# Optimization experiments

Measured on AMD Instinct MI355X. Metric: run time of the kernel, lower is better.

## Reference

```python
import jax, jax.numpy as jnp
import numpy as np

N1, E1 = 102400, 300000
N2, E2 = 10240, 40960
N3, E3 = 1024, 4096
G = 64
D = 256   # node_dim == hidden_dim (forced by where(M==0, x, M))
B = 64    # bond_dim
DEPTHS = (3, 3, 4)


def _make_edges(rng, n_nodes, n_edges):
    # build mirrored directed edges so every edge has an exact reverse
    half = n_edges // 2
    u = rng.integers(0, n_nodes, half)
    v = rng.integers(0, n_nodes, half)
    src = np.concatenate([u, v])
    dst = np.concatenate([v, u])
    rev = np.concatenate([np.arange(half, n_edges), np.arange(0, half)])
    return np.stack([src, dst]).astype(np.int64), rev.astype(np.int64)


def _linear_params(key, fan_in, fan_out):
    k1, k2 = jax.random.split(key)
    s = 1.0 / np.sqrt(fan_in)
    W = jax.random.uniform(k1, (fan_in, fan_out), jnp.float32, -s, s)
    b = jax.random.uniform(k2, (fan_out,), jnp.float32, -s, s)
    return W, b


def setup_inputs() -> dict:
    rng = np.random.default_rng(0)
    key = jax.random.key(0)
    ks = jax.random.split(key, 16)

    ei1, rev1 = _make_edges(rng, N1, E1)
    ei2, rev2 = _make_edges(rng, N2, E2)
    ei3, rev3 = _make_edges(rng, N3, E3)

    inp = {
        "x": jax.random.normal(ks[0], (N1, D), jnp.float32),
        "edge_attr1": jax.random.normal(ks[1], (E1, B), jnp.float32),
        "edge_attr2": jax.random.normal(ks[2], (E2, B), jnp.float32),
        "edge_attr3": jax.random.normal(ks[3], (E3, B), jnp.float32),
        "edge_index1": jnp.asarray(ei1), "rev_edge_index1": jnp.asarray(rev1),
        "edge_index2": jnp.asarray(ei2), "rev_edge_index2": jnp.asarray(rev2),
        "edge_index3": jnp.asarray(ei3), "rev_edge_index3": jnp.asarray(rev3),
        "batch1_2": jnp.asarray(np.repeat(np.arange(N2), N1 // N2)),
        "batch2": jnp.asarray(np.repeat(np.arange(N3), N2 // N3)),
        "batch3": jnp.asarray(np.repeat(np.arange(G), N3 // G)),
    }
    kidx = 4
    for lvl in (1, 2, 3):
        Wi, bi = _linear_params(ks[kidx], D + B, D); kidx += 1
        Wh, bh = _linear_params(ks[kidx], D, D); kidx += 1
        Wo, bo = _linear_params(ks[kidx], D + D, D); kidx += 1
        inp[f"Wi{lvl}"], inp[f"bi{lvl}"] = Wi, bi
        inp[f"Wh{lvl}"], inp[f"bh{lvl}"] = Wh, bh
        inp[f"Wo{lvl}"], inp[f"bo{lvl}"] = Wo, bo
    return inp


def _bmp(x, src, dst, rev, ea, Wi, bi, Wh, bh, Wo, bo, depth):
    # BondMessagePassing.forward (dropout is identity in eval)
    n = x.shape[0]
    H0 = jax.nn.relu(jnp.concatenate([x[src], ea], axis=1) @ Wi + bi)  # [E, D]
    H = H0
    for _ in range(depth - 1):
        agg = jax.ops.segment_sum(H, dst, num_segments=n)              # [N, D]
        M = agg[src] - H[rev]
        H = jax.nn.relu(H0 + M @ Wh + bh)
    M = jax.ops.segment_sum(H, dst, num_segments=n)
    M = jnp.where(jnp.sum(M, axis=1, keepdims=True) == 0, x, M)
    return jax.nn.relu(jnp.concatenate([x, M], axis=1) @ Wo + bo)


def _mean_pool(h, seg, n):
    s = jax.ops.segment_sum(h, seg, num_segments=n)
    c = jax.ops.segment_sum(jnp.ones((h.shape[0], 1), h.dtype), seg, num_segments=n)
    return s / jnp.maximum(c, 1.0)


def reference(x, edge_attr1, edge_attr2, edge_attr3,
              edge_index1, rev_edge_index1, edge_index2, rev_edge_index2,
              edge_index3, rev_edge_index3, batch1_2, batch2, batch3,
              Wi1, bi1, Wh1, bh1, Wo1, bo1,
              Wi2, bi2, Wh2, bh2, Wo2, bo2,
              Wi3, bi3, Wh3, bh3, Wo3, bo3):
    h1 = _bmp(x, edge_index1[0], edge_index1[1], rev_edge_index1, edge_attr1,
              Wi1, bi1, Wh1, bh1, Wo1, bo1, DEPTHS[0])
    x2 = _mean_pool(h1, batch1_2, N2)
    h2 = _bmp(x2, edge_index2[0], edge_index2[1], rev_edge_index2, edge_attr2,
              Wi2, bi2, Wh2, bh2, Wo2, bo2, DEPTHS[1])
    x3 = _mean_pool(h2, batch2, N3)
    h3 = _bmp(x3, edge_index3[0], edge_index3[1], rev_edge_index3, edge_attr3,
              Wi3, bi3, Wh3, bh3, Wo3, bo3, DEPTHS[2])
    out = _mean_pool(h3, batch3, G)  # [G, D] subgraph3_pooled
    return out
```

## Files before the change

### kernel.cpp

```cpp
#include <hip/hip_runtime.h>
#include <stdint.h>

typedef __bf16 bf16;
typedef __bf16 bf16x4 __attribute__((ext_vector_type(4)));
typedef __bf16 bf16x8 __attribute__((ext_vector_type(8)));
typedef float  f32x4  __attribute__((ext_vector_type(4)));

__device__ __forceinline__ int clampi(int v, int n) { return (v < 0 || v >= n) ? 0 : v; }

__global__ void cvt_kernel(const float* __restrict__ in, bf16* __restrict__ out, int n8) {
  int i = blockIdx.x * 256 + threadIdx.x;
  if (i >= n8) return;
  float4 a = ((const float4*)in)[i * 2];
  float4 b = ((const float4*)in)[i * 2 + 1];
  bf16x8 o = {(bf16)a.x, (bf16)a.y, (bf16)a.z, (bf16)a.w,
              (bf16)b.x, (bf16)b.y, (bf16)b.z, (bf16)b.w};
  ((bf16x8*)out)[i] = o;
}

__global__ void wtcvt_kernel(const float* __restrict__ W, bf16* __restrict__ Wt, int K) {
  int idx = blockIdx.x * 256 + threadIdx.x;
  if (idx >= K * 256) return;
  int k = idx >> 8, n = idx & 255;
  Wt[(size_t)n * K + k] = (bf16)W[idx];
}

__global__ void hist_kernel(const int* __restrict__ dst, int E, int* __restrict__ cnt, int N) {
  int e = blockIdx.x * 256 + threadIdx.x;
  if (e < E) atomicAdd(&cnt[clampi(dst[e], N)], 1);
}

__global__ void scan_block_kernel(const int* __restrict__ cnt, int N,
                                  int* __restrict__ incl, int* __restrict__ bsums) {
  __shared__ int sd[256];
  int t = threadIdx.x, bid = blockIdx.x;
  int base = bid * 1024 + t * 4;
  int v0 = (base + 0 < N) ? cnt[base + 0] : 0;
  int v1 = (base + 1 < N) ? cnt[base + 1] : 0;
  int v2 = (base + 2 < N) ? cnt[base + 2] : 0;
  int v3 = (base + 3 < N) ? cnt[base + 3] : 0;
  int s1 = v0 + v1, s2 = s1 + v2, s3 = s2 + v3;
  sd[t] = s3;
  __syncthreads();
  for (int off = 1; off < 256; off <<= 1) {
    int x = 0;
    if (t >= off) x = sd[t - off];
    __syncthreads();
    sd[t] += x;
    __syncthreads();
  }
  int excl = sd[t] - s3;
  if (base + 0 < N) incl[base + 0] = excl + v0;
  if (base + 1 < N) incl[base + 1] = excl + s1;
  if (base + 2 < N) incl[base + 2] = excl + s2;
  if (base + 3 < N) incl[base + 3] = excl + s3;
  if (t == 255) bsums[bid] = sd[255];
}

__global__ void scan_sums_kernel(const int* __restrict__ bsums, int nb, int* __restrict__ bexcl) {
  __shared__ int sd[256];
  int t = threadIdx.x;
  int v = (t < nb) ? bsums[t] : 0;
  sd[t] = v;
  __syncthreads();
  for (int off = 1; off < 256; off <<= 1) {
    int x = 0;
    if (t >= off) x = sd[t - off];
    __syncthreads();
    sd[t] += x;
    __syncthreads();
  }
  if (t < nb) bexcl[t] = sd[t] - v;
}

__global__ void scan_add_kernel(const int* __restrict__ incl, const int* __restrict__ bexcl,
                                int N, int* __restrict__ offs) {
  int i = blockIdx.x * 256 + threadIdx.x;
  if (i < N) offs[i + 1] = incl[i] + bexcl[i >> 10];
  if (i == 0) offs[0] = 0;
}

__global__ void scatter_kernel(const int* __restrict__ dst, int E, const int* __restrict__ offs,
                               int* __restrict__ cursor, int* __restrict__ elist, int N) {
  int e = blockIdx.x * 256 + threadIdx.x;
  if (e < E) {
    int d = clampi(dst[e], N);
    int p = atomicAdd(&cursor[d], 1);
    elist[offs[d] + p] = e;
  }
}

template <int WHERE, int XF32>
__global__ void segsum_kernel(const bf16* __restrict__ H, const int* __restrict__ elist,
                              const int* __restrict__ offs, const float* __restrict__ xf,
                              const bf16* __restrict__ xb, bf16* __restrict__ out, int N) {
  int lane = threadIdx.x & 63;
  int node = blockIdx.x * 4 + (threadIdx.x >> 6);
  if (node >= N) return;
  int beg = offs[node], end = offs[node + 1];
  float a0 = 0.f, a1 = 0.f, a2 = 0.f, a3 = 0.f;
  for (int p = beg; p < end; ++p) {
    int e = elist[p];
    bf16x4 v = ((const bf16x4*)(H + (size_t)e * 256))[lane];
    a0 += (float)v[0]; a1 += (float)v[1]; a2 += (float)v[2]; a3 += (float)v[3];
  }
  if (WHERE) {
    float s = a0 + a1 + a2 + a3;
    for (int off = 1; off < 64; off <<= 1) s += __shfl_xor(s, off);
    if (s == 0.f) {
      bf16x4 o;
      if (XF32) {
        float4 xv = ((const float4*)(xf))[(size_t)node * 64 + lane];
        o[0] = (bf16)xv.x; o[1] = (bf16)xv.y; o[2] = (bf16)xv.z; o[3] = (bf16)xv.w;
      } else {
        o = ((const bf16x4*)(xb + (size_t)node * 256))[lane];
      }
      ((bf16x4*)(out + (size_t)node * 256))[lane] = o;
      return;
    }
  }
  bf16x4 o = {(bf16)a0, (bf16)a1, (bf16)a2, (bf16)a3};
  ((bf16x4*)(out + (size_t)node * 256))[lane] = o;
}

template <int OUTF32>
__global__ void pool_kernel(const bf16* __restrict__ h, bf16* __restrict__ outb,
                            float* __restrict__ outf, int Nout, int cnt) {
  int lane = threadIdx.x & 63;
  int node = blockIdx.x * 4 + (threadIdx.x >> 6);
  if (node >= Nout) return;
  float a0 = 0.f, a1 = 0.f, a2 = 0.f, a3 = 0.f;
  size_t base = (size_t)node * cnt;
  for (int p = 0; p < cnt; ++p) {
    bf16x4 v = ((const bf16x4*)(h + (base + p) * 256))[lane];
    a0 += (float)v[0]; a1 += (float)v[1]; a2 += (float)v[2]; a3 += (float)v[3];
  }
  float c = (float)cnt;
  a0 /= c; a1 /= c; a2 /= c; a3 /= c;
  if (OUTF32) {
    float4 o = {a0, a1, a2, a3};
    ((float4*)(outf + (size_t)node * 256))[lane] = o;
  } else {
    bf16x4 o = {(bf16)a0, (bf16)a1, (bf16)a2, (bf16)a3};
    ((bf16x4*)(outb + (size_t)node * 256))[lane] = o;
  }
}

template <int MODE, int XF32>
__global__ __launch_bounds__(512) void gemm_kernel(
    const float* __restrict__ A1f, const bf16* __restrict__ A1b,
    const float* __restrict__ A2f, const bf16* __restrict__ A2b,
    const bf16* __restrict__ Wt, const float* __restrict__ bias, const bf16* H0,
    const int* __restrict__ srcIdx, const int* __restrict__ revIdx,
    bf16* out, int Mrows, int Nsrc) {
  constexpr int KK = MODE == 0 ? 320 : (MODE == 1 ? 256 : 512);
  constexpr int NK = KK / 64;
  __shared__ __align__(16) bf16 As[2][64 * 64];
  const int tid = threadIdx.x;
  const int lane = tid & 63;
  const int wave = tid >> 6;
  const int wm = wave >> 2, wn = wave & 3;
  const int m0 = blockIdx.x * 64;

  const int rowA = tid >> 3, uA = tid & 7;
  int base1, base2;
  {
    int rr = m0 + rowA;
    if (rr >= Mrows) rr = Mrows - 1;
    if (MODE == 0) {
      base1 = clampi(srcIdx[rr], Nsrc) * 256;
      base2 = rr * 64;
    } else if (MODE == 1) {
      base1 = clampi(srcIdx[rr], Nsrc) * 256;
      base2 = clampi(revIdx[rr], Mrows) * 256;
    } else {
      base1 = rr * 256;
      base2 = rr * 256;
    }
  }
  int colE[4];
#pragma unroll
  for (int j = 0; j < 4; ++j) colE[j] = (wn * 64 + j * 16 + (lane & 15)) * KK;

  f32x4 acc[2][4];
#pragma unroll
  for (int i = 0; i < 2; ++i)
#pragma unroll
    for (int j = 0; j < 4; ++j) acc[i][j] = (f32x4){0.f, 0.f, 0.f, 0.f};

  float4 pf[2];

  auto loadA = [&](int kc) {
    int k0 = kc * 64, u8 = uA * 8;
    if (MODE == 0) {
      if (k0 < 256) {
        if (XF32) {
          const float* g = A1f + (size_t)(base1 + k0 + u8);
          pf[0] = *(const float4*)g;
          pf[1] = *(const float4*)(g + 4);
        } else {
          pf[0] = *(const float4*)(A1b + (size_t)(base1 + k0 + u8));
        }
      } else {
        const float* g = A2f + (size_t)(base2 + u8);
        pf[0] = *(const float4*)g;
        pf[1] = *(const float4*)(g + 4);
      }
    } else if (MODE == 1) {
      pf[0] = *(const float4*)(A1b + (size_t)(base1 + k0 + u8));
      pf[1] = *(const float4*)(A2b + (size_t)(base2 + k0 + u8));
    } else {
      if (k0 < 256) {
        if (XF32) {
          const float* g = A1f + (size_t)(base1 + k0 + u8);
          pf[0] = *(const float4*)g;
          pf[1] = *(const float4*)(g + 4);
        } else {
          pf[0] = *(const float4*)(A1b + (size_t)(base1 + k0 + u8));
        }
      } else {
        pf[0] = *(const float4*)(A2b + (size_t)(base2 + (k0 - 256) + u8));
      }
    }
  };

  auto writeA = [&](int kc, int buf) {
    int k0 = kc * 64;
    int us = uA ^ (rowA & 7);
    bf16x8 v;
    bool cvt32;
    if (MODE == 0) cvt32 = XF32 || (k0 >= 256);
    else if (MODE == 2) cvt32 = XF32 && (k0 < 256);
    else cvt32 = false;
    if (MODE == 1) {
      bf16x8 va = *(bf16x8*)&pf[0];
      bf16x8 vh = *(bf16x8*)&pf[1];
#pragma unroll
      for (int j = 0; j < 8; ++j) v[j] = (bf16)((float)va[j] - (float)vh[j]);
    } else if (cvt32) {
      const float* f = (const float*)&pf[0];
#pragma unroll
      for (int j = 0; j < 8; ++j) v[j] = (bf16)f[j];
    } else {
      v = *(bf16x8*)&pf[0];
    }
    *(bf16x8*)(&As[buf][((size_t)rowA * 8 + us) * 8]) = v;
  };

  auto compute = [&](int kc, int buf) {
    const bf16* Asb = As[buf];
#pragma unroll
    for (int s = 0; s < 2; ++s) {
      int kq = s * 4 + (lane >> 4);
      int boff = kc * 64 + kq * 8;
      bf16x8 bfr[4];
#pragma unroll
      for (int j = 0; j < 4; ++j) bfr[j] = *(const bf16x8*)(Wt + (size_t)(colE[j] + boff));
      bf16x8 af[2];
#pragma unroll
      for (int i = 0; i < 2; ++i) {
        int ar = wm * 32 + i * 16 + (lane & 15);
        af[i] = *(const bf16x8*)(&Asb[(size_t)ar * 64 + (size_t)(kq ^ (ar & 7)) * 8]);
      }
#pragma unroll
      for (int i = 0; i < 2; ++i)
#pragma unroll
        for (int j = 0; j < 4; ++j)
          acc[i][j] = __builtin_amdgcn_mfma_f32_16x16x32_bf16(af[i], bfr[j], acc[i][j], 0, 0, 0);
    }
  };

  loadA(0);
  writeA(0, 0);
  __syncthreads();
#pragma unroll
  for (int kc = 0; kc < NK; ++kc) {
    if (kc + 1 < NK) loadA(kc + 1);
    compute(kc, kc & 1);
    if (kc + 1 < NK) writeA(kc + 1, (kc + 1) & 1);
    __syncthreads();
  }
#pragma unroll
  for (int i = 0; i < 2; ++i) {
    int rbase = m0 + wm * 32 + i * 16 + ((lane >> 4) << 2);
#pragma unroll
    for (int j = 0; j < 4; ++j) {
      int col = wn * 64 + j * 16 + (lane & 15);
      float bcol = bias[col];
#pragma unroll
      for (int r = 0; r < 4; ++r) {
        int row = rbase + r;
        if (row < Mrows) {
          float v = acc[i][j][r] + bcol;
          if (MODE == 1) v += (float)H0[(size_t)row * 256 + col];
          v = fmaxf(v, 0.f);
          out[(size_t)row * 256 + col] = (bf16)v;
        }
      }
    }
  }
}

template <int XF32>
static void run_level(const float* xf, const bf16* xb, const float* ea,
                      const int* src, const int* dst, const int* rev, int E, int N, int depth,
                      const bf16* WiT, const float* bi_, const bf16* WhT, const float* bh_,
                      const bf16* WoT, const float* bo_,
                      bf16* C, bf16* Dd, bf16* Ee, bf16* agg, bf16* h,
                      int* cnt, int* incl, int* offs, int* cursr, int* bsums, int* bexcl,
                      int* elist, hipStream_t stream) {
  hipMemsetAsync(cnt, 0, (size_t)N * 4, stream);
  hist_kernel<<<(E + 255) / 256, 256, 0, stream>>>(dst, E, cnt, N);
  int nb = (N + 1023) / 1024;
  scan_block_kernel<<<nb, 256, 0, stream>>>(cnt, N, incl, bsums);
  scan_sums_kernel<<<1, 256, 0, stream>>>(bsums, nb, bexcl);
  scan_add_kernel<<<(N + 255) / 256, 256, 0, stream>>>(incl, bexcl, N, offs);
  hipMemsetAsync(cursr, 0, (size_t)N * 4, stream);
  scatter_kernel<<<(E + 255) / 256, 256, 0, stream>>>(dst, E, offs, cursr, elist, N);

  dim3 ge((E + 63) / 64);
  gemm_kernel<0, XF32><<<ge, 512, 0, stream>>>(xf, xb, ea, nullptr, WiT, bi_, nullptr, src,
                                               nullptr, C, E, N);
  bf16* Hcur = C;
  for (int it = 0; it < depth - 1; ++it) {
    segsum_kernel<0, 0><<<(N + 3) / 4, 256, 0, stream>>>(Hcur, elist, offs, nullptr, nullptr,
                                                         agg, N);
    bf16* Hn = (it == depth - 2) ? C : ((it & 1) ? Ee : Dd);
    gemm_kernel<1, 0><<<ge, 512, 0, stream>>>(nullptr, agg, nullptr, Hcur, WhT, bh_, C, src,
                                              rev, Hn, E, N);
    Hcur = Hn;
  }
  segsum_kernel<1, XF32><<<(N + 3) / 4, 256, 0, stream>>>(Hcur, elist, offs, xf, xb, agg, N);
  dim3 gn((N + 63) / 64);
  gemm_kernel<2, XF32><<<gn, 512, 0, stream>>>(xf, xb, nullptr, agg, WoT, bo_, nullptr, nullptr,
                                               nullptr, h, N, N);
}

extern "C" void kernel_launch(void* const* d_in, const int* in_sizes, int n_in,
                              void* d_out, int out_size, void* d_ws, size_t ws_size,
                              hipStream_t stream) {
  constexpr int N1 = 102400, E1 = 300000;
  constexpr int N2 = 10240, E2 = 40960;
  constexpr int N3 = 1024, E3 = 4096;
  constexpr int G = 64;
  constexpr int KI = 320, KH = 256, KO = 512;

  const float* x   = (const float*)d_in[0];
  const float* ea1 = (const float*)d_in[1];
  const float* ea2 = (const float*)d_in[2];
  const float* ea3 = (const float*)d_in[3];
  const int* ei1 = (const int*)d_in[4];
  const int* rv1 = (const int*)d_in[5];
  const int* ei2 = (const int*)d_in[6];
  const int* rv2 = (const int*)d_in[7];
  const int* ei3 = (const int*)d_in[8];
  const int* rv3 = (const int*)d_in[9];
  const float *Wi[3], *bi[3], *Wh[3], *bh[3], *Wo[3], *bo[3];
  for (int l = 0; l < 3; ++l) {
    Wi[l] = (const float*)d_in[13 + 6 * l + 0];
    bi[l] = (const float*)d_in[13 + 6 * l + 1];
    Wh[l] = (const float*)d_in[13 + 6 * l + 2];
    bh[l] = (const float*)d_in[13 + 6 * l + 3];
    Wo[l] = (const float*)d_in[13 + 6 * l + 4];
    bo[l] = (const float*)d_in[13 + 6 * l + 5];
  }
  float* outp = (float*)d_out;
  char* ws = (char*)d_ws;

  size_t off = 0;
  auto alloc = [&](size_t b) { size_t o = off; off += (b + 255) & ~(size_t)255; return o; };
  size_t o_wit[3], o_wht[3], o_wot[3];
  for (int l = 0; l < 3; ++l) {
    o_wit[l] = alloc((size_t)256 * KI * 2);
    o_wht[l] = alloc((size_t)256 * KH * 2);
    o_wot[l] = alloc((size_t)256 * KO * 2);
  }
  size_t o_C   = alloc((size_t)E1 * 256 * 2);
  size_t o_D   = alloc((size_t)E1 * 256 * 2);
  size_t o_E3b = alloc((size_t)E3 * 256 * 2);
  size_t o_agg = alloc((size_t)N1 * 256 * 2);
  size_t o_x2  = alloc((size_t)N2 * 256 * 2);
  size_t o_h2  = alloc((size_t)N2 * 256 * 2);
  size_t o_x3  = alloc((size_t)N3 * 256 * 2);
  size_t o_h3  = alloc((size_t)N3 * 256 * 2);
  size_t o_cnt = alloc((size_t)N1 * 4);
  size_t o_inc = alloc((size_t)N1 * 4);
  size_t o_off = alloc((size_t)(N1 + 1) * 4);
  size_t o_cur = alloc((size_t)N1 * 4);
  size_t o_bs  = alloc(1024 * 4);
  size_t o_bx  = alloc(1024 * 4);
  size_t o_el  = alloc((size_t)E1 * 4);
  size_t need_base = off;
  size_t o_xb = alloc((size_t)N1 * 256 * 2);
  size_t need_ext = off;

  if (ws_size < need_base) {
    hipMemsetAsync(d_out, 0, (size_t)out_size * 4, stream);
    return;
  }
  const bool use_xb = (ws_size >= need_ext);

  int* cnt   = (int*)(ws + o_cnt);
  int* incl  = (int*)(ws + o_inc);
  int* offs  = (int*)(ws + o_off);
  int* cursr = (int*)(ws + o_cur);
  int* bsums = (int*)(ws + o_bs);
  int* bexcl = (int*)(ws + o_bx);
  int* elist = (int*)(ws + o_el);
  bf16* C    = (bf16*)(ws + o_C);
  bf16* Dd   = (bf16*)(ws + o_D);
  bf16* E3b  = (bf16*)(ws + o_E3b);
  bf16* agg  = (bf16*)(ws + o_agg);
  bf16* x2b  = (bf16*)(ws + o_x2);
  bf16* h2b  = (bf16*)(ws + o_h2);
  bf16* x3b  = (bf16*)(ws + o_x3);
  bf16* h3b  = (bf16*)(ws + o_h3);
  bf16* xbp  = (bf16*)(ws + o_xb);

  for (int l = 0; l < 3; ++l) {
    wtcvt_kernel<<<(KI * 256 + 255) / 256, 256, 0, stream>>>(Wi[l], (bf16*)(ws + o_wit[l]), KI);
    wtcvt_kernel<<<(KH * 256 + 255) / 256, 256, 0, stream>>>(Wh[l], (bf16*)(ws + o_wht[l]), KH);
    wtcvt_kernel<<<(KO * 256 + 255) / 256, 256, 0, stream>>>(Wo[l], (bf16*)(ws + o_wot[l]), KO);
  }

  if (use_xb) {
    cvt_kernel<<<(N1 * 256 / 8 + 255) / 256, 256, 0, stream>>>(x, xbp, N1 * 256 / 8);
    run_level<0>(nullptr, xbp, ea1, ei1, ei1 + E1, rv1, E1, N1, 3,
                 (bf16*)(ws + o_wit[0]), bi[0], (bf16*)(ws + o_wht[0]), bh[0],
                 (bf16*)(ws + o_wot[0]), bo[0], C, Dd, Dd, agg, C,
                 cnt, incl, offs, cursr, bsums, bexcl, elist, stream);
  } else {
    run_level<1>(x, nullptr, ea1, ei1, ei1 + E1, rv1, E1, N1, 3,
                 (bf16*)(ws + o_wit[0]), bi[0], (bf16*)(ws + o_wht[0]), bh[0],
                 (bf16*)(ws + o_wot[0]), bo[0], C, Dd, Dd, agg, C,
                 cnt, incl, offs, cursr, bsums, bexcl, elist, stream);
  }
  pool_kernel<0><<<(N2 + 3) / 4, 256, 0, stream>>>(C, x2b, nullptr, N2, N1 / N2);

  run_level<0>(nullptr, x2b, ea2, ei2, ei2 + E2, rv2, E2, N2, 3,
               (bf16*)(ws + o_wit[1]), bi[1], (bf16*)(ws + o_wht[1]), bh[1],
               (bf16*)(ws + o_wot[1]), bo[1], C, Dd, Dd, agg, h2b,
               cnt, incl, offs, cursr, bsums, bexcl, elist, stream);
  pool_kernel<0><<<(N3 + 3) / 4, 256, 0, stream>>>(h2b, x3b, nullptr, N3, N2 / N3);

  run_level<0>(nullptr, x3b, ea3, ei3, ei3 + E3, rv3, E3, N3, 4,
               (bf16*)(ws + o_wit[2]), bi[2], (bf16*)(ws + o_wht[2]), bh[2],
               (bf16*)(ws + o_wot[2]), bo[2], C, Dd, E3b, agg, h3b,
               cnt, incl, offs, cursr, bsums, bexcl, elist, stream);
  pool_kernel<1><<<(G + 3) / 4, 256, 0, stream>>>(h3b, nullptr, outp, G, N3 / G);
}
```

Before: 1.516 ms.

## Preload full gathered A rows into LDS for edge GEMMs

Result: slower. 1.570 ms (+3.6%).

```diff
diff --git a/kernel.cpp b/kernel.cpp
--- a/kernel.cpp
+++ b/kernel.cpp
@@ -147,14 +147,150 @@
 }
 
 template <int MODE, int XF32>
-__global__ __launch_bounds__(512) void gemm_kernel(
+__global__ __launch_bounds__(512) void gemm_gather(
     const float* __restrict__ A1f, const bf16* __restrict__ A1b,
-    const float* __restrict__ A2f, const bf16* __restrict__ A2b,
+    const float* __restrict__ eaf, const bf16* __restrict__ Hrv,
     const bf16* __restrict__ Wt, const float* __restrict__ bias, const bf16* H0,
     const int* __restrict__ srcIdx, const int* __restrict__ revIdx,
     bf16* out, int Mrows, int Nsrc) {
-  constexpr int KK = MODE == 0 ? 320 : (MODE == 1 ? 256 : 512);
+  constexpr int KK = (MODE == 0) ? 320 : 256;
   constexpr int NK = KK / 64;
+  __shared__ __align__(16) bf16 As[64 * 256];
+  __shared__ __align__(16) bf16 A2s[(MODE == 0) ? 64 * 64 : 64];
+  const int tid = threadIdx.x;
+  const int lane = tid & 63;
+  const int wave = tid >> 6;
+  const int wm = wave >> 2, wn = wave & 3;
+  const int m0 = blockIdx.x * 64;
+
+  const int rowA = tid >> 3, lane8 = tid & 7;
+  {
+    int rr = m0 + rowA;
+    if (rr >= Mrows) rr = Mrows - 1;
+    if (MODE == 0) {
+      int sn = clampi(srcIdx[rr], Nsrc);
+      int swz = lane8 ^ (rowA & 7);
+      if (XF32) {
+        const float* gx = A1f + (size_t)sn * 256;
+        float4 p[4][2];
+#pragma unroll
+        for (int st = 0; st < 4; ++st) {
+          const float* g = gx + (lane8 + 8 * st) * 8;
+          p[st][0] = *(const float4*)g;
+          p[st][1] = *(const float4*)(g + 4);
+        }
+#pragma unroll
+        for (int st = 0; st < 4; ++st) {
+          const float* f = (const float*)&p[st][0];
+          bf16x8 v;
+#pragma unroll
+          for (int j = 0; j < 8; ++j) v[j] = (bf16)f[j];
+          *(bf16x8*)(&As[((size_t)rowA * 32 + 8 * st + swz) * 8]) = v;
+        }
+      } else {
+        const bf16* gx = A1b + (size_t)sn * 256;
+        float4 p[4];
+#pragma unroll
+        for (int st = 0; st < 4; ++st) p[st] = *(const float4*)(gx + (lane8 + 8 * st) * 8);
+#pragma unroll
+        for (int st = 0; st < 4; ++st)
+          *(bf16x8*)(&As[((size_t)rowA * 32 + 8 * st + swz) * 8]) = *(bf16x8*)&p[st];
+      }
+      const float* ge = eaf + (size_t)rr * 64 + lane8 * 8;
+      float4 e0 = *(const float4*)ge, e1 = *(const float4*)(ge + 4);
+      bf16x8 ev = {(bf16)e0.x, (bf16)e0.y, (bf16)e0.z, (bf16)e0.w,
+                   (bf16)e1.x, (bf16)e1.y, (bf16)e1.z, (bf16)e1.w};
+      *(bf16x8*)(&A2s[((size_t)rowA * 8 + swz) * 8]) = ev;
+    } else {
+      int sn = clampi(srcIdx[rr], Nsrc);
+      int rv = clampi(revIdx[rr], Mrows);
+      const bf16* ga = A1b + (size_t)sn * 256;
+      const bf16* gh = Hrv + (size_t)rv * 256;
+      float4 pa[4], ph[4];
+#pragma unroll
+      for (int st = 0; st < 4; ++st) {
+        pa[st] = *(const float4*)(ga + (lane8 + 8 * st) * 8);
+        ph[st] = *(const float4*)(gh + (lane8 + 8 * st) * 8);
+      }
+      int swz = lane8 ^ (rowA & 7);
+#pragma unroll
+      for (int st = 0; st < 4; ++st) {
+        bf16x8 va = *(bf16x8*)&pa[st];
+        bf16x8 vh = *(bf16x8*)&ph[st];
+        bf16x8 v;
+#pragma unroll
+        for (int j = 0; j < 8; ++j) v[j] = (bf16)((float)va[j] - (float)vh[j]);
+        *(bf16x8*)(&As[((size_t)rowA * 32 + 8 * st + swz) * 8]) = v;
+      }
+    }
+  }
+
+  f32x4 acc[2][4];
+#pragma unroll
+  for (int i = 0; i < 2; ++i)
+#pragma unroll
+    for (int j = 0; j < 4; ++j) acc[i][j] = (f32x4){0.f, 0.f, 0.f, 0.f};
+
+  int colE[4];
+#pragma unroll
+  for (int j = 0; j < 4; ++j) colE[j] = (wn * 64 + j * 16 + (lane & 15)) * KK;
+
+  __syncthreads();
+
+#pragma unroll
+  for (int kc = 0; kc < NK; ++kc) {
+#pragma unroll
+    for (int s = 0; s < 2; ++s) {
+      int kq = s * 4 + (lane >> 4);
+      int boff = kc * 64 + kq * 8;
+      bf16x8 bfr[4];
+#pragma unroll
+      for (int j = 0; j < 4; ++j) bfr[j] = *(const bf16x8*)(Wt + (size_t)(colE[j] + boff));
+      bf16x8 af[2];
+#pragma unroll
+      for (int i = 0; i < 2; ++i) {
+        int ar = wm * 32 + i * 16 + (lane & 15);
+        if (MODE == 0 && kc == NK - 1) {
+          af[i] = *(const bf16x8*)(&A2s[((size_t)ar * 8 + (kq ^ (ar & 7))) * 8]);
+        } else {
+          af[i] = *(const bf16x8*)(&As[((size_t)ar * 32 + kc * 8 + (kq ^ (ar & 7))) * 8]);
+        }
+      }
+#pragma unroll
+      for (int i = 0; i < 2; ++i)
+#pragma unroll
+        for (int j = 0; j < 4; ++j)
+          acc[i][j] = __builtin_amdgcn_mfma_f32_16x16x32_bf16(af[i], bfr[j], acc[i][j], 0, 0, 0);
+    }
+  }
+#pragma unroll
+  for (int i = 0; i < 2; ++i) {
+    int rbase = m0 + wm * 32 + i * 16 + ((lane >> 4) << 2);
+#pragma unroll
+    for (int j = 0; j < 4; ++j) {
+      int col = wn * 64 + j * 16 + (lane & 15);
+      float bcol = bias[col];
+#pragma unroll
+      for (int r = 0; r < 4; ++r) {
+        int row = rbase + r;
+        if (row < Mrows) {
+          float v = acc[i][j][r] + bcol;
+          if (MODE == 1) v += (float)H0[(size_t)row * 256 + col];
+          v = fmaxf(v, 0.f);
+          out[(size_t)row * 256 + col] = (bf16)v;
+        }
+      }
+    }
+  }
+}
+
+template <int XF32>
+__global__ __launch_bounds__(512) void gemm_stream(
+    const float* __restrict__ A1f, const bf16* __restrict__ A1b, const bf16* __restrict__ A2b,
+    const bf16* __restrict__ Wt, const float* __restrict__ bias,
+    bf16* __restrict__ out, int Mrows) {
+  constexpr int KK = 512;
+  constexpr int NK = 8;
   __shared__ __align__(16) bf16 As[2][64 * 64];
   const int tid = threadIdx.x;
   const int lane = tid & 63;
@@ -163,20 +299,11 @@
   const int m0 = blockIdx.x * 64;
 
   const int rowA = tid >> 3, uA = tid & 7;
-  int base1, base2;
+  int rbase;
   {
     int rr = m0 + rowA;
     if (rr >= Mrows) rr = Mrows - 1;
-    if (MODE == 0) {
-      base1 = clampi(srcIdx[rr], Nsrc) * 256;
-      base2 = rr * 64;
-    } else if (MODE == 1) {
-      base1 = clampi(srcIdx[rr], Nsrc) * 256;
-      base2 = clampi(revIdx[rr], Mrows) * 256;
-    } else {
-      base1 = rr * 256;
-      base2 = rr * 256;
-    }
+    rbase = rr * 256;
   }
   int colE[4];
 #pragma unroll
@@ -189,55 +316,25 @@
     for (int j = 0; j < 4; ++j) acc[i][j] = (f32x4){0.f, 0.f, 0.f, 0.f};
 
   float4 pf[2];
-
   auto loadA = [&](int kc) {
     int k0 = kc * 64, u8 = uA * 8;
-    if (MODE == 0) {
-      if (k0 < 256) {
-        if (XF32) {
-          const float* g = A1f + (size_t)(base1 + k0 + u8);
-          pf[0] = *(const float4*)g;
-          pf[1] = *(const float4*)(g + 4);
-        } else {
-          pf[0] = *(const float4*)(A1b + (size_t)(base1 + k0 + u8));
-        }
-      } else {
-        const float* g = A2f + (size_t)(base2 + u8);
+    if (k0 < 256) {
+      if (XF32) {
+        const float* g = A1f + (size_t)(rbase + k0 + u8);
         pf[0] = *(const float4*)g;
         pf[1] = *(const float4*)(g + 4);
-      }
-    } else if (MODE == 1) {
-      pf[0] = *(const float4*)(A1b + (size_t)(base1 + k0 + u8));
-      pf[1] = *(const float4*)(A2b + (size_t)(base2 + k0 + u8));
+      } else {
+        pf[0] = *(const float4*)(A1b + (size_t)(rbase + k0 + u8));
+      }
     } else {
-      if (k0 < 256) {
-        if (XF32) {
-          const float* g = A1f + (size_t)(base1 + k0 + u8);
-          pf[0] = *(const float4*)g;
-          pf[1] = *(const float4*)(g + 4);
-        } else {
-          pf[0] = *(const float4*)(A1b + (size_t)(base1 + k0 + u8));
-        }
-      } else {
-        pf[0] = *(const float4*)(A2b + (size_t)(base2 + (k0 - 256) + u8));
-      }
+      pf[0] = *(const float4*)(A2b + (size_t)(rbase + (k0 - 256) + u8));
     }
   };
-
   auto writeA = [&](int kc, int buf) {
     int k0 = kc * 64;
     int us = uA ^ (rowA & 7);
     bf16x8 v;
-    bool cvt32;
-    if (MODE == 0) cvt32 = XF32 || (k0 >= 256);
-    else if (MODE == 2) cvt32 = XF32 && (k0 < 256);
-    else cvt32 = false;
-    if (MODE == 1) {
-      bf16x8 va = *(bf16x8*)&pf[0];
-      bf16x8 vh = *(bf16x8*)&pf[1];
-#pragma unroll
-      for (int j = 0; j < 8; ++j) v[j] = (bf16)((float)va[j] - (float)vh[j]);
-    } else if (cvt32) {
+    if (XF32 && k0 < 256) {
       const float* f = (const float*)&pf[0];
 #pragma unroll
       for (int j = 0; j < 8; ++j) v[j] = (bf16)f[j];
@@ -246,7 +343,6 @@
     }
     *(bf16x8*)(&As[buf][((size_t)rowA * 8 + us) * 8]) = v;
   };
-
   auto compute = [&](int kc, int buf) {
     const bf16* Asb = As[buf];
 #pragma unroll
@@ -282,18 +378,16 @@
   }
 #pragma unroll
   for (int i = 0; i < 2; ++i) {
-    int rbase = m0 + wm * 32 + i * 16 + ((lane >> 4) << 2);
+    int rb = m0 + wm * 32 + i * 16 + ((lane >> 4) << 2);
 #pragma unroll
     for (int j = 0; j < 4; ++j) {
       int col = wn * 64 + j * 16 + (lane & 15);
       float bcol = bias[col];
 #pragma unroll
       for (int r = 0; r < 4; ++r) {
-        int row = rbase + r;
+        int row = rb + r;
         if (row < Mrows) {
-          float v = acc[i][j][r] + bcol;
-          if (MODE == 1) v += (float)H0[(size_t)row * 256 + col];
-          v = fmaxf(v, 0.f);
+          float v = fmaxf(acc[i][j][r] + bcol, 0.f);
           out[(size_t)row * 256 + col] = (bf16)v;
         }
       }
@@ -319,21 +413,20 @@
   scatter_kernel<<<(E + 255) / 256, 256, 0, stream>>>(dst, E, offs, cursr, elist, N);
 
   dim3 ge((E + 63) / 64);
-  gemm_kernel<0, XF32><<<ge, 512, 0, stream>>>(xf, xb, ea, nullptr, WiT, bi_, nullptr, src,
+  gemm_gather<0, XF32><<<ge, 512, 0, stream>>>(xf, xb, ea, nullptr, WiT, bi_, nullptr, src,
                                                nullptr, C, E, N);
   bf16* Hcur = C;
   for (int it = 0; it < depth - 1; ++it) {
     segsum_kernel<0, 0><<<(N + 3) / 4, 256, 0, stream>>>(Hcur, elist, offs, nullptr, nullptr,
                                                          agg, N);
     bf16* Hn = (it == depth - 2) ? C : ((it & 1) ? Ee : Dd);
-    gemm_kernel<1, 0><<<ge, 512, 0, stream>>>(nullptr, agg, nullptr, Hcur, WhT, bh_, C, src,
+    gemm_gather<1, 0><<<ge, 512, 0, stream>>>(nullptr, agg, nullptr, Hcur, WhT, bh_, C, src,
                                               rev, Hn, E, N);
     Hcur = Hn;
   }
   segsum_kernel<1, XF32><<<(N + 3) / 4, 256, 0, stream>>>(Hcur, elist, offs, xf, xb, agg, N);
   dim3 gn((N + 63) / 64);
-  gemm_kernel<2, XF32><<<gn, 512, 0, stream>>>(xf, xb, nullptr, agg, WoT, bo_, nullptr, nullptr,
-                                               nullptr, h, N, N);
+  gemm_stream<XF32><<<gn, 512, 0, stream>>>(xf, xb, agg, WoT, bo_, h, N);
 }
 
 extern "C" void kernel_launch(void* const* d_in, const int* in_sizes, int n_in,
```
